# Kernel optimization log

Measured on AMD Instinct MI355X. Metric: run time of the kernel, lower is better.

Reference implementation:

```python
import math
import jax, jax.numpy as jnp
import numpy as np

SEQ_LEN = 2048
PATCH = 16
D_MODEL = 512
N_HEADS = 8
D_FF = 2048
E_LAYERS = 3
KERNELS = (8, 4, 2, 1)


def _pos_embedding(L, d):
    # standard sinusoidal PE, matches PositionalEmbedding
    pos = np.arange(L, dtype=np.float32)[:, None]
    div = np.exp(np.arange(0, d, 2, dtype=np.float32) * (-math.log(10000.0) / d))
    pe = np.zeros((L, d), dtype=np.float32)
    pe[:, 0::2] = np.sin(pos * div)
    pe[:, 1::2] = np.cos(pos * div)
    return jnp.asarray(pe)


def _layer_norm(x, g, b, eps=1e-5):
    mu = jnp.mean(x, axis=-1, keepdims=True)
    var = jnp.mean(jnp.square(x - mu), axis=-1, keepdims=True)
    return (x - mu) * jax.lax.rsqrt(var + eps) * g + b


def setup_inputs() -> dict:
    key = jax.random.key(0)
    ks = jax.random.split(key, 12)
    bs, c = 8, 32
    s = 0.02
    L, D = E_LAYERS, D_MODEL
    inp = {
        "x_enc": jax.random.normal(ks[0], (bs, SEQ_LEN, c), jnp.float32),
        "W_emb": jax.random.normal(ks[1], (PATCH, D), jnp.float32) * s,
        "Wq": jax.random.normal(ks[2], (L, D, D), jnp.float32) * s,
        "bq": jnp.zeros((L, D), jnp.float32),
        "Wk": jax.random.normal(ks[3], (L, D, D), jnp.float32) * s,
        "bk": jnp.zeros((L, D), jnp.float32),
        "Wv": jax.random.normal(ks[4], (L, D, D), jnp.float32) * s,
        "bv": jnp.zeros((L, D), jnp.float32),
        "Wo": jax.random.normal(ks[5], (L, D, D), jnp.float32) * s,
        "bo": jnp.zeros((L, D), jnp.float32),
        "ln1_g": jnp.ones((L, D), jnp.float32),
        "ln1_b": jnp.zeros((L, D), jnp.float32),
        "W1": jax.random.normal(ks[6], (L, D, D_FF), jnp.float32) * s,
        "b1": jnp.zeros((L, D_FF), jnp.float32),
        "W2": jax.random.normal(ks[7], (L, D_FF, D), jnp.float32) * s,
        "b2": jnp.zeros((L, D), jnp.float32),
        "ln2_g": jnp.ones((L, D), jnp.float32),
        "ln2_b": jnp.zeros((L, D), jnp.float32),
        "lnf_g": jnp.ones((D,), jnp.float32),
        "lnf_b": jnp.zeros((D,), jnp.float32),
    }
    return inp


def reference(x_enc, W_emb, Wq, bq, Wk, bk, Wv, bv, Wo, bo,
              ln1_g, ln1_b, W1, b1, W2, b2, ln2_g, ln2_b, lnf_g, lnf_b):
    bs, t, c = x_enc.shape
    B = bs * c
    # channel-independent sequences: (bs, t, c) -> (bs*c, t)
    x = jnp.transpose(x_enc, (0, 2, 1)).reshape(B, t)

    # multi-scale interval sampling + patch embedding per scale
    p_lens = [(t // k) // PATCH for k in KERNELS]  # [16, 32, 64, 128]
    toks = []
    for k in KERNELS:
        xs = x[:, ::k]  # interval sampling (replicate-pad unfold [...,0] == stride-k sampling here)
        patches = xs.reshape(B, -1, PATCH)  # non-overlapping patches (stride == patch_len)
        toks.append(patches @ W_emb)  # value embedding, no bias
    h = jnp.concatenate(toks, axis=1)  # (B, L_tot=240, D)

    # multi-scale positional embedding: downsample pe of finest scale
    pe = _pos_embedding(p_lens[-1], D_MODEL)
    pos = jnp.concatenate([pe[::k] for k in KERNELS], axis=0)  # (240, D)
    h = h + pos[None]

    # block-diagonal scale-independence mask
    seg = np.concatenate([np.full(pl, i, dtype=np.int32) for i, pl in enumerate(p_lens)])
    allowed = jnp.asarray(seg[:, None] == seg[None, :])  # (240, 240) True = attend

    hd = D_MODEL // N_HEADS
    scale = 1.0 / math.sqrt(hd)
    Ltot = h.shape[1]
    for i in range(E_LAYERS):
        q = (h @ Wq[i] + bq[i]).reshape(B, Ltot, N_HEADS, hd)
        k_ = (h @ Wk[i] + bk[i]).reshape(B, Ltot, N_HEADS, hd)
        v_ = (h @ Wv[i] + bv[i]).reshape(B, Ltot, N_HEADS, hd)
        scores = jnp.einsum('blhd,bmhd->bhlm', q, k_) * scale
        scores = jnp.where(allowed[None, None], scores, -jnp.inf)
        attn = jax.nn.softmax(scores, axis=-1)
        o = jnp.einsum('bhlm,bmhd->blhd', attn, v_).reshape(B, Ltot, D_MODEL)
        o = o @ Wo[i] + bo[i]
        h = _layer_norm(h + o, ln1_g[i], ln1_b[i])
        f = jax.nn.gelu(h @ W1[i] + b1[i]) @ W2[i] + b2[i]
        h = _layer_norm(h + f, ln2_g[i], ln2_b[i])
    return _layer_norm(h, lnf_g, lnf_b)
```

## Files before the change

### kernel.cpp

```cpp
#include <hip/hip_runtime.h>
#include <hip/hip_bf16.h>

typedef short bf16x8 __attribute__((ext_vector_type(8)));
typedef float f32x4 __attribute__((ext_vector_type(4)));
using bf16 = __hip_bfloat16;

#define GLOBAL_LOAD_LDS16(g, l)                                                          \
    __builtin_amdgcn_global_load_lds((const __attribute__((address_space(1))) unsigned int*)(g), \
                                     (__attribute__((address_space(3))) unsigned int*)(l), \
                                     16, 0, 0)

static __device__ __forceinline__ float gelu_f(float x) {
    float u = 1.5957691216057308f * x * (1.0f + 0.044715f * x * x);
    return x / (1.0f + __expf(-u));
}

static __device__ __forceinline__ unsigned pack_bf16(float lo, float hi) {
    union { bf16 h; unsigned short u; } a, b;
    a.h = __float2bfloat16(lo);
    b.h = __float2bfloat16(hi);
    return ((unsigned)b.u << 16) | (unsigned)a.u;
}

__global__ __launch_bounds__(256) void transpose_f32_bf16(const float* __restrict__ in,
                                                          bf16* __restrict__ out,
                                                          int R, int C, size_t zso) {
    __shared__ float tile[32][33];
    size_t zi = (size_t)blockIdx.z * R * C;
    size_t zo = (size_t)blockIdx.z * zso;
    int c0 = blockIdx.x * 32, r0 = blockIdx.y * 32;
    int tx = threadIdx.x & 31, ty = threadIdx.x >> 5;
    #pragma unroll
    for (int i = 0; i < 32; i += 8) {
        int r = r0 + ty + i, c = c0 + tx;
        if (r < R && c < C) tile[ty + i][tx] = in[zi + (size_t)r * C + c];
    }
    __syncthreads();
    #pragma unroll
    for (int i = 0; i < 32; i += 8) {
        int c = c0 + ty + i, r = r0 + tx;
        if (c < C && r < R) out[zo + (size_t)c * R + r] = __float2bfloat16(tile[tx][ty + i]);
    }
}

__global__ __launch_bounds__(256) void concat_bias(const float* __restrict__ bq,
                                                   const float* __restrict__ bk,
                                                   const float* __restrict__ bv,
                                                   float* __restrict__ out) {
    int i = blockIdx.x * 256 + threadIdx.x;
    if (i < 3 * 1536) {
        int L = i / 1536, r = i - L * 1536;
        float v = (r < 512) ? bq[L * 512 + r]
                : (r < 1024) ? bk[L * 512 + r - 512]
                             : bv[L * 512 + r - 1024];
        out[i] = v;
    }
}

__global__ __launch_bounds__(256) void transpose_v(const bf16* __restrict__ in,
                                                   bf16* __restrict__ out) {
    __shared__ bf16 tile[32][33];
    int b = blockIdx.z;
    int d0 = blockIdx.x * 32, t0 = blockIdx.y * 32;
    int tx = threadIdx.x & 31, ty = threadIdx.x >> 5;
    #pragma unroll
    for (int i = 0; i < 32; i += 8) {
        int tt = t0 + ty + i, dd = d0 + tx;
        if (tt < 240) tile[ty + i][tx] = in[((size_t)b * 240 + tt) * 1536 + 1024 + dd];
    }
    __syncthreads();
    #pragma unroll
    for (int i = 0; i < 32; i += 8) {
        int dd = d0 + ty + i, tt = t0 + tx;
        if (tt < 240) out[((size_t)b * 512 + dd) * 240 + tt] = tile[tx][ty + i];
    }
}

__global__ __launch_bounds__(256) void embed_kernel(const float* __restrict__ x_enc,
                                                    const float* __restrict__ W_emb,
                                                    bf16* __restrict__ h) {
    int row = blockIdx.x;
    int b = row / 240, l = row - b * 240;
    int s = (l < 16) ? 0 : (l < 48) ? 1 : (l < 112) ? 2 : 3;
    int len = 16 << s;
    int off = len - 16;
    int kk = 8 >> s;
    int j = l - off;
    int bs_i = b >> 5, c_i = b & 31;
    __shared__ float xv[16];
    int t = threadIdx.x;
    if (t < 16) {
        int tau = (j * 16 + t) * kk;
        xv[t] = x_enc[((size_t)bs_i * 2048 + tau) * 32 + c_i];
    }
    __syncthreads();
    int pe_row = j * kk;
    const float NEG2LN = -0.035977892078032f;
    for (int d = t; d < 512; d += 256) {
        float acc = 0.f;
        #pragma unroll
        for (int i = 0; i < 16; ++i) acc += xv[i] * W_emb[i * 512 + d];
        int di = d >> 1;
        float ang = (float)pe_row * expf((float)di * NEG2LN);
        float pos = (d & 1) ? cosf(ang) : sinf(ang);
        h[(size_t)row * 512 + d] = __float2bfloat16(acc + pos);
    }
}

__global__ __launch_bounds__(512, 2) void gemm_bt_256(const bf16* __restrict__ A,
                                                      const bf16* __restrict__ Bt,
                                                      const float* __restrict__ bias,
                                                      bf16* __restrict__ C,
                                                      int M, int N, int K, int act) {
    __shared__ __align__(16) bf16 smem[2 * 32768];
    const int t = threadIdx.x;
    const int wave = t >> 6, lane = t & 63;
    const int quad = lane >> 4, l16 = lane & 15;
    const int axor = l16 & 7;

    const int nwg = gridDim.x * gridDim.y;
    const int id = blockIdx.y * gridDim.x + blockIdx.x;
    const int swz = (id & 7) * (nwg >> 3) + (id >> 3);
    const int bx = swz % gridDim.x, by = swz / gridDim.x;
    const int m0 = by * 256, n0 = bx * 256;

    const int wm = (wave >> 2) * 128;
    const int wn = (wave & 3) * 64;

    f32x4 acc[8][4];
    #pragma unroll
    for (int a = 0; a < 8; ++a)
        #pragma unroll
        for (int b = 0; b < 4; ++b)
            #pragma unroll
            for (int r = 0; r < 4; ++r) acc[a][b][r] = 0.0f;

    const int srow = lane >> 3;
    const int schunk = (lane & 7) ^ srow;
    const bf16* Abase = A + (size_t)(m0 + wave * 32 + srow) * K + schunk * 8;
    const bf16* Bbase = Bt + (size_t)(n0 + wave * 32 + srow) * K + schunk * 8;

    #pragma unroll
    for (int p = 0; p < 4; ++p)
        GLOBAL_LOAD_LDS16(Abase + (size_t)(p * 8) * K, smem + (wave * 4 + p) * 512);
    #pragma unroll
    for (int p = 0; p < 4; ++p)
        GLOBAL_LOAD_LDS16(Bbase + (size_t)(p * 8) * K, smem + 16384 + (wave * 4 + p) * 512);

    bf16x8 af[4][2], b0[2][2], b1[2][2];

#define BARRIER() asm volatile("s_barrier" ::: "memory")
#define LOAD_A(mq)                                                                    \
    _Pragma("unroll")                                                                 \
    for (int mi = 0; mi < 4; ++mi)                                                    \
        _Pragma("unroll")                                                             \
        for (int kk = 0; kk < 2; ++kk)                                                \
            af[mi][kk] = *(const bf16x8*)&Asl[(wm + (mq) * 64 + mi * 16 + l16) * 64   \
                                              + (((kk << 2) + quad) ^ axor) * 8];
#define LOAD_B(nq, dst)                                                               \
    _Pragma("unroll")                                                                 \
    for (int ni = 0; ni < 2; ++ni)                                                    \
        _Pragma("unroll")                                                             \
        for (int kk = 0; kk < 2; ++kk)                                                \
            dst[ni][kk] = *(const bf16x8*)&Bsl[(wn + (nq) * 32 + ni * 16 + l16) * 64  \
                                               + (((kk << 2) + quad) ^ axor) * 8];
#define MMA_Q(mo, no, src)                                                            \
    __builtin_amdgcn_s_setprio(1);                                                    \
    _Pragma("unroll")                                                                 \
    for (int mi = 0; mi < 4; ++mi)                                                    \
        _Pragma("unroll")                                                             \
        for (int ni = 0; ni < 2; ++ni)                                                \
            _Pragma("unroll")                                                         \
            for (int kk = 0; kk < 2; ++kk)                                            \
                acc[(mo) + mi][(no) + ni] = __builtin_amdgcn_mfma_f32_16x16x32_bf16(  \
                    af[mi][kk], src[ni][kk], acc[(mo) + mi][(no) + ni], 0, 0, 0);     \
    __builtin_amdgcn_s_setprio(0);

    const int NK = K >> 6;
    for (int kt = 0; kt < NK - 1; ++kt) {
        const int s = kt & 1;
        const bf16* Asl = smem + s * 32768;
        const bf16* Bsl = Asl + 16384;
        bf16* Asn = smem + (s ^ 1) * 32768;
        bf16* Bsn = Asn + 16384;
        const size_t kn = (size_t)(kt + 1) << 6;
        #pragma unroll
        for (int p = 0; p < 4; ++p)
            GLOBAL_LOAD_LDS16(Abase + (size_t)(p * 8) * K + kn, Asn + (wave * 4 + p) * 512);
        asm volatile("s_waitcnt vmcnt(4)" ::: "memory");
        BARRIER();
        LOAD_A(0); LOAD_B(0, b0);
        GLOBAL_LOAD_LDS16(Bbase + kn, Bsn + (wave * 4 + 0) * 512);
        GLOBAL_LOAD_LDS16(Bbase + (size_t)8 * K + kn, Bsn + (wave * 4 + 1) * 512);
        MMA_Q(0, 0, b0);
        BARRIER();
        LOAD_B(1, b1);
        GLOBAL_LOAD_LDS16(Bbase + (size_t)16 * K + kn, Bsn + (wave * 4 + 2) * 512);
        GLOBAL_LOAD_LDS16(Bbase + (size_t)24 * K + kn, Bsn + (wave * 4 + 3) * 512);
        MMA_Q(0, 2, b1);
        BARRIER();
        LOAD_A(1);
        MMA_Q(4, 0, b0);
        BARRIER();
        MMA_Q(4, 2, b1);
    }
    {
        const bf16* Asl = smem + ((NK - 1) & 1) * 32768;
        const bf16* Bsl = Asl + 16384;
        asm volatile("s_waitcnt vmcnt(0)" ::: "memory");
        BARRIER();
        LOAD_A(0); LOAD_B(0, b0);
        MMA_Q(0, 0, b0);
        BARRIER();
        LOAD_B(1, b1);
        MMA_Q(0, 2, b1);
        BARRIER();
        LOAD_A(1);
        MMA_Q(4, 0, b0);
        BARRIER();
        MMA_Q(4, 2, b1);
    }
#undef BARRIER
#undef LOAD_A
#undef LOAD_B
#undef MMA_Q

    {
        char* ctile = (char*)smem;
        const int oddl = l16 & 1;
        #pragma unroll
        for (int ni = 0; ni < 4; ++ni) {
            int colt = wn + ni * 16 + l16;
            float bv = bias[n0 + colt];
            #pragma unroll
            for (int mi = 0; mi < 8; ++mi) {
                float v0 = acc[mi][ni][0] + bv;
                float v1 = acc[mi][ni][1] + bv;
                float v2 = acc[mi][ni][2] + bv;
                float v3 = acc[mi][ni][3] + bv;
                if (act) {
                    v0 = gelu_f(v0); v1 = gelu_f(v1);
                    v2 = gelu_f(v2); v3 = gelu_f(v3);
                }
                float p0 = __shfl_xor(v0, 1);
                float p1 = __shfl_xor(v1, 1);
                float p2 = __shfl_xor(v2, 1);
                float p3 = __shfl_xor(v3, 1);
                float lo0 = oddl ? p1 : v0, hi0 = oddl ? v1 : p0;
                float lo1 = oddl ? p3 : v2, hi1 = oddl ? v3 : p2;
                int rowt0 = wm + mi * 16 + quad * 4 + oddl;
                int rowt1 = rowt0 + 2;
                int colp = colt & ~1;
                *(unsigned*)(ctile + rowt0 * 512 + ((((colp >> 3) ^ (rowt0 & 31)) << 4) | ((colp & 7) << 1)))
                    = pack_bf16(lo0, hi0);
                *(unsigned*)(ctile + rowt1 * 512 + ((((colp >> 3) ^ (rowt1 & 31)) << 4) | ((colp & 7) << 1)))
                    = pack_bf16(lo1, hi1);
            }
        }
        __syncthreads();
        const int rsub = t >> 5;
        const int cch = t & 31;
        #pragma unroll
        for (int g = 0; g < 16; ++g) {
            int row = g * 16 + rsub;
            bf16x8 v = *(const bf16x8*)(ctile + row * 512 + ((cch ^ (row & 31)) << 4));
            *(bf16x8*)(C + (size_t)(m0 + row) * N + n0 + cch * 8) = v;
        }
    }
}

template<int LEN>
__global__ __launch_bounds__(256) void attn_mfma(const bf16* __restrict__ qkv,
                                                 const bf16* __restrict__ vt,
                                                 bf16* __restrict__ o) {
    constexpr int NT = LEN / 16;
    constexpr int KT = (LEN >= 32) ? (LEN / 32) : 1;
    constexpr int PST = (LEN == 16) ? 40 : (LEN + 8);
    constexpr int SLABS = LEN / 16;
    constexpr int OFF = LEN - 16;
    __shared__ __align__(16) bf16 Plds[4 * 16 * PST];

    const int t = threadIdx.x;
    const int wave = t >> 6, lane = t & 63;
    const int quad = lane >> 4, l16 = lane & 15;
    const int task = blockIdx.x * 4 + wave;
    const int b = task / (8 * SLABS);
    const int rem = task - b * (8 * SLABS);
    const int h = rem / SLABS;
    const int slab = rem - h * SLABS;

    const size_t qbase = ((size_t)b * 240 + OFF) * 1536 + h * 64;
    const size_t obase = ((size_t)b * 240 + OFF) * 512 + h * 64;

    const bf16* qp = qkv + qbase + (size_t)(slab * 16 + l16) * 1536 + quad * 8;
    bf16x8 qf0 = *(const bf16x8*)qp;
    bf16x8 qf1 = *(const bf16x8*)(qp + 32);

    f32x4 sacc[NT];
    #pragma unroll
    for (int nt = 0; nt < NT; ++nt) {
        const bf16* kp = qkv + qbase + 512 + (size_t)(nt * 16 + l16) * 1536 + quad * 8;
        bf16x8 kf0 = *(const bf16x8*)kp;
        bf16x8 kf1 = *(const bf16x8*)(kp + 32);
        f32x4 a = {0.f, 0.f, 0.f, 0.f};
        a = __builtin_amdgcn_mfma_f32_16x16x32_bf16(qf0, kf0, a, 0, 0, 0);
        a = __builtin_amdgcn_mfma_f32_16x16x32_bf16(qf1, kf1, a, 0, 0, 0);
        sacc[nt] = a;
    }

    float mx[4], sm[4];
    #pragma unroll
    for (int r = 0; r < 4; ++r) mx[r] = -3.0e38f;
    #pragma unroll
    for (int nt = 0; nt < NT; ++nt)
        #pragma unroll
        for (int r = 0; r < 4; ++r) {
            sacc[nt][r] *= 0.125f;
            mx[r] = fmaxf(mx[r], sacc[nt][r]);
        }
    #pragma unroll
    for (int msk = 1; msk < 16; msk <<= 1)
        #pragma unroll
        for (int r = 0; r < 4; ++r) mx[r] = fmaxf(mx[r], __shfl_xor(mx[r], msk));
    #pragma unroll
    for (int r = 0; r < 4; ++r) sm[r] = 0.f;
    #pragma unroll
    for (int nt = 0; nt < NT; ++nt)
        #pragma unroll
        for (int r = 0; r < 4; ++r) {
            float p = __expf(sacc[nt][r] - mx[r]);
            sacc[nt][r] = p;
            sm[r] += p;
        }
    #pragma unroll
    for (int msk = 1; msk < 16; msk <<= 1)
        #pragma unroll
        for (int r = 0; r < 4; ++r) sm[r] += __shfl_xor(sm[r], msk);
    float inv[4];
    #pragma unroll
    for (int r = 0; r < 4; ++r) inv[r] = 1.f / sm[r];

    bf16* pw = Plds + wave * 16 * PST;
    #pragma unroll
    for (int nt = 0; nt < NT; ++nt)
        #pragma unroll
        for (int r = 0; r < 4; ++r)
            pw[(quad * 4 + r) * PST + nt * 16 + l16] =
                __float2bfloat16(sacc[nt][r] * inv[r]);
    if (LEN == 16) {
        #pragma unroll
        for (int r = 0; r < 4; ++r)
            pw[(quad * 4 + r) * PST + 16 + l16] = __float2bfloat16(0.f);
    }
    __syncthreads();

    f32x4 oacc[4];
    #pragma unroll
    for (int n4 = 0; n4 < 4; ++n4) {
        f32x4 z = {0.f, 0.f, 0.f, 0.f};
        oacc[n4] = z;
    }
    #pragma unroll
    for (int kt = 0; kt < KT; ++kt) {
        bf16x8 pf = *(const bf16x8*)&pw[l16 * PST + kt * 32 + quad * 8];
        #pragma unroll
        for (int n4 = 0; n4 < 4; ++n4) {
            const bf16* vp = vt + ((size_t)b * 512 + h * 64 + n4 * 16 + l16) * 240
                              + OFF + kt * 32 + quad * 8;
            bf16x8 vf = *(const bf16x8*)vp;
            oacc[n4] = __builtin_amdgcn_mfma_f32_16x16x32_bf16(pf, vf, oacc[n4], 0, 0, 0);
        }
    }
    #pragma unroll
    for (int n4 = 0; n4 < 4; ++n4)
        #pragma unroll
        for (int r = 0; r < 4; ++r)
            o[obase + (size_t)(slab * 16 + quad * 4 + r) * 512 + n4 * 16 + l16] =
                __float2bfloat16(oacc[n4][r]);
}

__global__ __launch_bounds__(256) void ln_kernel(const bf16* x, const bf16* res,
                                                 const float* __restrict__ g,
                                                 const float* __restrict__ bta,
                                                 bf16* out_bf, float* out_f) {
    int row = blockIdx.x;
    int t = threadIdx.x;
    const bf16* xr = x + (size_t)row * 512;
    float v0 = __bfloat162float(xr[t]);
    float v1 = __bfloat162float(xr[t + 256]);
    if (res) {
        const bf16* rr = res + (size_t)row * 512;
        v0 += __bfloat162float(rr[t]);
        v1 += __bfloat162float(rr[t + 256]);
    }
    float s = v0 + v1, ss = v0 * v0 + v1 * v1;
    #pragma unroll
    for (int mk = 1; mk < 64; mk <<= 1) { s += __shfl_xor(s, mk); ss += __shfl_xor(ss, mk); }
    __shared__ float red[8];
    int wave = t >> 6, lane = t & 63;
    if (lane == 0) { red[wave * 2] = s; red[wave * 2 + 1] = ss; }
    __syncthreads();
    s = red[0] + red[2] + red[4] + red[6];
    ss = red[1] + red[3] + red[5] + red[7];
    float mu = s * (1.f / 512.f);
    float var = ss * (1.f / 512.f) - mu * mu;
    float inv = rsqrtf(var + 1e-5f);
    float y0 = (v0 - mu) * inv * g[t] + bta[t];
    float y1 = (v1 - mu) * inv * g[t + 256] + bta[t + 256];
    if (out_bf) {
        bf16* orow = out_bf + (size_t)row * 512;
        orow[t] = __float2bfloat16(y0);
        orow[t + 256] = __float2bfloat16(y1);
    } else {
        float* orow = out_f + (size_t)row * 512;
        orow[t] = y0;
        orow[t + 256] = y1;
    }
}

extern "C" void kernel_launch(void* const* d_in, const int* in_sizes, int n_in,
                              void* d_out, int out_size, void* d_ws, size_t ws_size,
                              hipStream_t stream) {
    const float* x_enc = (const float*)d_in[0];
    const float* W_emb = (const float*)d_in[1];
    const float* Wq    = (const float*)d_in[2];
    const float* bq    = (const float*)d_in[3];
    const float* Wk    = (const float*)d_in[4];
    const float* bk    = (const float*)d_in[5];
    const float* Wv    = (const float*)d_in[6];
    const float* bv    = (const float*)d_in[7];
    const float* Wo    = (const float*)d_in[8];
    const float* bo    = (const float*)d_in[9];
    const float* ln1_g = (const float*)d_in[10];
    const float* ln1_b = (const float*)d_in[11];
    const float* W1    = (const float*)d_in[12];
    const float* b1    = (const float*)d_in[13];
    const float* W2    = (const float*)d_in[14];
    const float* b2    = (const float*)d_in[15];
    const float* ln2_g = (const float*)d_in[16];
    const float* ln2_b = (const float*)d_in[17];
    const float* lnf_g = (const float*)d_in[18];
    const float* lnf_b = (const float*)d_in[19];

    const int ROWS = 256 * 240;
    char* ws = (char*)d_ws;
    const size_t Hb = (size_t)ROWS * 512 * 2;
    bf16* h    = (bf16*)(ws);
    bf16* qkv  = (bf16*)(ws + Hb);
    bf16* oa   = (bf16*)(ws + 4 * Hb);
    bf16* scr2 = (bf16*)(ws + 5 * Hb);
    bf16* mid  = qkv;
    bf16* WqkvT = (bf16*)(ws + 6 * Hb);
    bf16* WoT  = WqkvT + (size_t)3 * 1536 * 512;
    bf16* W1T  = WoT + (size_t)3 * 512 * 512;
    bf16* W2T  = W1T + (size_t)3 * 512 * 2048;
    float* bcat = (float*)(W2T + (size_t)3 * 2048 * 512);

    bf16* vt     = scr2;
    bf16* oproj  = scr2;
    bf16* ffnout = scr2;

    dim3 blk(256);
    dim3 gblk(512);
    transpose_f32_bf16<<<dim3(16, 16, 3), blk, 0, stream>>>(Wq, WqkvT, 512, 512, (size_t)1536 * 512);
    transpose_f32_bf16<<<dim3(16, 16, 3), blk, 0, stream>>>(Wk, WqkvT + (size_t)512 * 512, 512, 512, (size_t)1536 * 512);
    transpose_f32_bf16<<<dim3(16, 16, 3), blk, 0, stream>>>(Wv, WqkvT + (size_t)1024 * 512, 512, 512, (size_t)1536 * 512);
    transpose_f32_bf16<<<dim3(16, 16, 3), blk, 0, stream>>>(Wo, WoT, 512, 512, (size_t)512 * 512);
    transpose_f32_bf16<<<dim3(64, 16, 3), blk, 0, stream>>>(W1, W1T, 512, 2048, (size_t)512 * 2048);
    transpose_f32_bf16<<<dim3(16, 64, 3), blk, 0, stream>>>(W2, W2T, 2048, 512, (size_t)2048 * 512);
    concat_bias<<<18, blk, 0, stream>>>(bq, bk, bv, bcat);

    embed_kernel<<<ROWS, blk, 0, stream>>>(x_enc, W_emb, h);

    for (int L = 0; L < 3; ++L) {
        size_t wo = (size_t)L * 512 * 512;
        size_t w1o = (size_t)L * 512 * 2048;
        gemm_bt_256<<<dim3(6, 240), gblk, 0, stream>>>(h, WqkvT + (size_t)L * 1536 * 512,
                                                       bcat + L * 1536, qkv, ROWS, 1536, 512, 0);
        transpose_v<<<dim3(16, 8, 256), blk, 0, stream>>>(qkv, vt);
        attn_mfma<16><<<512, blk, 0, stream>>>(qkv, vt, oa);
        attn_mfma<32><<<1024, blk, 0, stream>>>(qkv, vt, oa);
        attn_mfma<64><<<2048, blk, 0, stream>>>(qkv, vt, oa);
        attn_mfma<128><<<4096, blk, 0, stream>>>(qkv, vt, oa);
        gemm_bt_256<<<dim3(2, 240), gblk, 0, stream>>>(oa, WoT + wo, bo + L * 512, oproj, ROWS, 512, 512, 0);
        ln_kernel<<<ROWS, blk, 0, stream>>>(h, oproj, ln1_g + L * 512, ln1_b + L * 512, h, nullptr);
        gemm_bt_256<<<dim3(8, 240), gblk, 0, stream>>>(h, W1T + w1o, b1 + L * 2048, mid, ROWS, 2048, 512, 1);
        gemm_bt_256<<<dim3(2, 240), gblk, 0, stream>>>(mid, W2T + w1o, b2 + L * 512, ffnout, ROWS, 512, 2048, 0);
        ln_kernel<<<ROWS, blk, 0, stream>>>(h, ffnout, ln2_g + L * 512, ln2_b + L * 512, h, nullptr);
    }
    ln_kernel<<<ROWS, blk, 0, stream>>>(h, nullptr, lnf_g, lnf_b, nullptr, (float*)d_out);
}
```

Measured before the change: 2.735 ms.

## Replace 256x256 pipelined GEMM with simpler 128x128 single-buffered GEMM

Swaps the 512-thread 256x256 double-buffered GEMM, which interleaves global-to-LDS prefetch with MFMA, for a 256-thread 128x128 kernel. The new kernel loads each K-tile synchronously, then computes on it. The epilogue swizzle is adapted to the narrower tile with a new row permutation. This trades lower LDS use and finer grid granularity for losing load/compute overlap and reducing data reuse per tile.

```diff
diff --git a/kernel.cpp b/kernel.cpp
--- a/kernel.cpp
+++ b/kernel.cpp
@@ -20,6 +20,10 @@
     a.h = __float2bfloat16(lo);
     b.h = __float2bfloat16(hi);
     return ((unsigned)b.u << 16) | (unsigned)a.u;
+}
+
+static __device__ __forceinline__ int eperm(int r) {
+    return (r & 1) | (((r >> 2) & 3) << 1) | (((r >> 1) & 1) << 3);
 }
 
 __global__ __launch_bounds__(256) void transpose_f32_bf16(const float* __restrict__ in,
@@ -107,29 +111,28 @@
     }
 }
 
-__global__ __launch_bounds__(512, 2) void gemm_bt_256(const bf16* __restrict__ A,
-                                                      const bf16* __restrict__ Bt,
-                                                      const float* __restrict__ bias,
-                                                      bf16* __restrict__ C,
-                                                      int M, int N, int K, int act) {
-    __shared__ __align__(16) bf16 smem[2 * 32768];
+__global__ __launch_bounds__(256) void gemm_bt(const bf16* __restrict__ A,
+                                               const bf16* __restrict__ Bt,
+                                               const float* __restrict__ bias,
+                                               bf16* __restrict__ C,
+                                               int M, int N, int K, int act) {
+    __shared__ __align__(16) bf16 smem[2 * 128 * 64];
+    bf16* As = smem;
+    bf16* Bs = smem + 128 * 64;
     const int t = threadIdx.x;
     const int wave = t >> 6, lane = t & 63;
     const int quad = lane >> 4, l16 = lane & 15;
-    const int axor = l16 & 7;
 
     const int nwg = gridDim.x * gridDim.y;
     const int id = blockIdx.y * gridDim.x + blockIdx.x;
-    const int swz = (id & 7) * (nwg >> 3) + (id >> 3);
-    const int bx = swz % gridDim.x, by = swz / gridDim.x;
-    const int m0 = by * 256, n0 = bx * 256;
-
-    const int wm = (wave >> 2) * 128;
-    const int wn = (wave & 3) * 64;
-
-    f32x4 acc[8][4];
-    #pragma unroll
-    for (int a = 0; a < 8; ++a)
+    const int swzb = (id & 7) * (nwg >> 3) + (id >> 3);
+    const int bx = swzb % gridDim.x, by = swzb / gridDim.x;
+    const int m0 = by * 128, n0 = bx * 128;
+    const int wm = (wave >> 1) * 64, wn = (wave & 1) * 64;
+
+    f32x4 acc[4][4];
+    #pragma unroll
+    for (int a = 0; a < 4; ++a)
         #pragma unroll
         for (int b = 0; b < 4; ++b)
             #pragma unroll
@@ -140,91 +143,37 @@
     const bf16* Abase = A + (size_t)(m0 + wave * 32 + srow) * K + schunk * 8;
     const bf16* Bbase = Bt + (size_t)(n0 + wave * 32 + srow) * K + schunk * 8;
 
-    #pragma unroll
-    for (int p = 0; p < 4; ++p)
-        GLOBAL_LOAD_LDS16(Abase + (size_t)(p * 8) * K, smem + (wave * 4 + p) * 512);
-    #pragma unroll
-    for (int p = 0; p < 4; ++p)
-        GLOBAL_LOAD_LDS16(Bbase + (size_t)(p * 8) * K, smem + 16384 + (wave * 4 + p) * 512);
-
-    bf16x8 af[4][2], b0[2][2], b1[2][2];
-
-#define BARRIER() asm volatile("s_barrier" ::: "memory")
-#define LOAD_A(mq)                                                                    \
-    _Pragma("unroll")                                                                 \
-    for (int mi = 0; mi < 4; ++mi)                                                    \
-        _Pragma("unroll")                                                             \
-        for (int kk = 0; kk < 2; ++kk)                                                \
-            af[mi][kk] = *(const bf16x8*)&Asl[(wm + (mq) * 64 + mi * 16 + l16) * 64   \
-                                              + (((kk << 2) + quad) ^ axor) * 8];
-#define LOAD_B(nq, dst)                                                               \
-    _Pragma("unroll")                                                                 \
-    for (int ni = 0; ni < 2; ++ni)                                                    \
-        _Pragma("unroll")                                                             \
-        for (int kk = 0; kk < 2; ++kk)                                                \
-            dst[ni][kk] = *(const bf16x8*)&Bsl[(wn + (nq) * 32 + ni * 16 + l16) * 64  \
-                                               + (((kk << 2) + quad) ^ axor) * 8];
-#define MMA_Q(mo, no, src)                                                            \
-    __builtin_amdgcn_s_setprio(1);                                                    \
-    _Pragma("unroll")                                                                 \
-    for (int mi = 0; mi < 4; ++mi)                                                    \
-        _Pragma("unroll")                                                             \
-        for (int ni = 0; ni < 2; ++ni)                                                \
-            _Pragma("unroll")                                                         \
-            for (int kk = 0; kk < 2; ++kk)                                            \
-                acc[(mo) + mi][(no) + ni] = __builtin_amdgcn_mfma_f32_16x16x32_bf16(  \
-                    af[mi][kk], src[ni][kk], acc[(mo) + mi][(no) + ni], 0, 0, 0);     \
-    __builtin_amdgcn_s_setprio(0);
-
-    const int NK = K >> 6;
-    for (int kt = 0; kt < NK - 1; ++kt) {
-        const int s = kt & 1;
-        const bf16* Asl = smem + s * 32768;
-        const bf16* Bsl = Asl + 16384;
-        bf16* Asn = smem + (s ^ 1) * 32768;
-        bf16* Bsn = Asn + 16384;
-        const size_t kn = (size_t)(kt + 1) << 6;
-        #pragma unroll
-        for (int p = 0; p < 4; ++p)
-            GLOBAL_LOAD_LDS16(Abase + (size_t)(p * 8) * K + kn, Asn + (wave * 4 + p) * 512);
-        asm volatile("s_waitcnt vmcnt(4)" ::: "memory");
-        BARRIER();
-        LOAD_A(0); LOAD_B(0, b0);
-        GLOBAL_LOAD_LDS16(Bbase + kn, Bsn + (wave * 4 + 0) * 512);
-        GLOBAL_LOAD_LDS16(Bbase + (size_t)8 * K + kn, Bsn + (wave * 4 + 1) * 512);
-        MMA_Q(0, 0, b0);
-        BARRIER();
-        LOAD_B(1, b1);
-        GLOBAL_LOAD_LDS16(Bbase + (size_t)16 * K + kn, Bsn + (wave * 4 + 2) * 512);
-        GLOBAL_LOAD_LDS16(Bbase + (size_t)24 * K + kn, Bsn + (wave * 4 + 3) * 512);
-        MMA_Q(0, 2, b1);
-        BARRIER();
-        LOAD_A(1);
-        MMA_Q(4, 0, b0);
-        BARRIER();
-        MMA_Q(4, 2, b1);
-    }
-    {
-        const bf16* Asl = smem + ((NK - 1) & 1) * 32768;
-        const bf16* Bsl = Asl + 16384;
-        asm volatile("s_waitcnt vmcnt(0)" ::: "memory");
-        BARRIER();
-        LOAD_A(0); LOAD_B(0, b0);
-        MMA_Q(0, 0, b0);
-        BARRIER();
-        LOAD_B(1, b1);
-        MMA_Q(0, 2, b1);
-        BARRIER();
-        LOAD_A(1);
-        MMA_Q(4, 0, b0);
-        BARRIER();
-        MMA_Q(4, 2, b1);
-    }
-#undef BARRIER
-#undef LOAD_A
-#undef LOAD_B
-#undef MMA_Q
-
+    for (int k0 = 0; k0 < K; k0 += 64) {
+        __syncthreads();
+        #pragma unroll
+        for (int p = 0; p < 4; ++p) {
+            GLOBAL_LOAD_LDS16(Abase + (size_t)p * 8 * K + k0, As + (wave * 4 + p) * 512);
+            GLOBAL_LOAD_LDS16(Bbase + (size_t)p * 8 * K + k0, Bs + (wave * 4 + p) * 512);
+        }
+        __syncthreads();
+        #pragma unroll
+        for (int kt = 0; kt < 2; ++kt) {
+            bf16x8 af[4], bfr[4];
+            #pragma unroll
+            for (int mi = 0; mi < 4; ++mi) {
+                int row = wm + mi * 16 + l16;
+                af[mi] = *(const bf16x8*)(&As[row * 64 + (((kt << 2) + quad) ^ (l16 & 7)) * 8]);
+            }
+            #pragma unroll
+            for (int ni = 0; ni < 4; ++ni) {
+                int row = wn + ni * 16 + l16;
+                bfr[ni] = *(const bf16x8*)(&Bs[row * 64 + (((kt << 2) + quad) ^ (l16 & 7)) * 8]);
+            }
+            #pragma unroll
+            for (int mi = 0; mi < 4; ++mi)
+                #pragma unroll
+                for (int ni = 0; ni < 4; ++ni)
+                    acc[mi][ni] = __builtin_amdgcn_mfma_f32_16x16x32_bf16(af[mi], bfr[ni],
+                                                                         acc[mi][ni], 0, 0, 0);
+        }
+    }
+
+    __syncthreads();
     {
         char* ctile = (char*)smem;
         const int oddl = l16 & 1;
@@ -233,7 +182,7 @@
             int colt = wn + ni * 16 + l16;
             float bv = bias[n0 + colt];
             #pragma unroll
-            for (int mi = 0; mi < 8; ++mi) {
+            for (int mi = 0; mi < 4; ++mi) {
                 float v0 = acc[mi][ni][0] + bv;
                 float v1 = acc[mi][ni][1] + bv;
                 float v2 = acc[mi][ni][2] + bv;
@@ -251,19 +200,20 @@
                 int rowt0 = wm + mi * 16 + quad * 4 + oddl;
                 int rowt1 = rowt0 + 2;
                 int colp = colt & ~1;
-                *(unsigned*)(ctile + rowt0 * 512 + ((((colp >> 3) ^ (rowt0 & 31)) << 4) | ((colp & 7) << 1)))
+                int ch = colp >> 3;
+                *(unsigned*)(ctile + rowt0 * 256 + (((ch ^ eperm(rowt0)) << 4) | ((colp & 7) << 1)))
                     = pack_bf16(lo0, hi0);
-                *(unsigned*)(ctile + rowt1 * 512 + ((((colp >> 3) ^ (rowt1 & 31)) << 4) | ((colp & 7) << 1)))
+                *(unsigned*)(ctile + rowt1 * 256 + (((ch ^ eperm(rowt1)) << 4) | ((colp & 7) << 1)))
                     = pack_bf16(lo1, hi1);
             }
         }
         __syncthreads();
-        const int rsub = t >> 5;
-        const int cch = t & 31;
-        #pragma unroll
-        for (int g = 0; g < 16; ++g) {
+        const int rsub = t >> 4;
+        const int cch = t & 15;
+        #pragma unroll
+        for (int g = 0; g < 8; ++g) {
             int row = g * 16 + rsub;
-            bf16x8 v = *(const bf16x8*)(ctile + row * 512 + ((cch ^ (row & 31)) << 4));
+            bf16x8 v = *(const bf16x8*)(ctile + row * 256 + ((cch ^ eperm(row)) << 4));
             *(bf16x8*)(C + (size_t)(m0 + row) * N + n0 + cch * 8) = v;
         }
     }
@@ -461,7 +411,6 @@
     bf16* ffnout = scr2;
 
     dim3 blk(256);
-    dim3 gblk(512);
     transpose_f32_bf16<<<dim3(16, 16, 3), blk, 0, stream>>>(Wq, WqkvT, 512, 512, (size_t)1536 * 512);
     transpose_f32_bf16<<<dim3(16, 16, 3), blk, 0, stream>>>(Wk, WqkvT + (size_t)512 * 512, 512, 512, (size_t)1536 * 512);
     transpose_f32_bf16<<<dim3(16, 16, 3), blk, 0, stream>>>(Wv, WqkvT + (size_t)1024 * 512, 512, 512, (size_t)1536 * 512);
@@ -475,17 +424,17 @@
     for (int L = 0; L < 3; ++L) {
         size_t wo = (size_t)L * 512 * 512;
         size_t w1o = (size_t)L * 512 * 2048;
-        gemm_bt_256<<<dim3(6, 240), gblk, 0, stream>>>(h, WqkvT + (size_t)L * 1536 * 512,
-                                                       bcat + L * 1536, qkv, ROWS, 1536, 512, 0);
+        gemm_bt<<<dim3(12, 480), blk, 0, stream>>>(h, WqkvT + (size_t)L * 1536 * 512,
+                                                   bcat + L * 1536, qkv, ROWS, 1536, 512, 0);
         transpose_v<<<dim3(16, 8, 256), blk, 0, stream>>>(qkv, vt);
         attn_mfma<16><<<512, blk, 0, stream>>>(qkv, vt, oa);
         attn_mfma<32><<<1024, blk, 0, stream>>>(qkv, vt, oa);
         attn_mfma<64><<<2048, blk, 0, stream>>>(qkv, vt, oa);
         attn_mfma<128><<<4096, blk, 0, stream>>>(qkv, vt, oa);
-        gemm_bt_256<<<dim3(2, 240), gblk, 0, stream>>>(oa, WoT + wo, bo + L * 512, oproj, ROWS, 512, 512, 0);
+        gemm_bt<<<dim3(4, 480), blk, 0, stream>>>(oa, WoT + wo, bo + L * 512, oproj, ROWS, 512, 512, 0);
         ln_kernel<<<ROWS, blk, 0, stream>>>(h, oproj, ln1_g + L * 512, ln1_b + L * 512, h, nullptr);
-        gemm_bt_256<<<dim3(8, 240), gblk, 0, stream>>>(h, W1T + w1o, b1 + L * 2048, mid, ROWS, 2048, 512, 1);
-        gemm_bt_256<<<dim3(2, 240), gblk, 0, stream>>>(mid, W2T + w1o, b2 + L * 512, ffnout, ROWS, 512, 2048, 0);
+        gemm_bt<<<dim3(16, 480), blk, 0, stream>>>(h, W1T + w1o, b1 + L * 2048, mid, ROWS, 2048, 512, 1);
+        gemm_bt<<<dim3(4, 480), blk, 0, stream>>>(mid, W2T + w1o, b2 + L * 512, ffnout, ROWS, 512, 2048, 0);
         ln_kernel<<<ROWS, blk, 0, stream>>>(h, ffnout, ln2_g + L * 512, ln2_b + L * 512, h, nullptr);
     }
     ln_kernel<<<ROWS, blk, 0, stream>>>(h, nullptr, lnf_g, lnf_b, nullptr, (float*)d_out);
```

After: 2.875 ms. 5.1% more time.
